# Optimization experiments

Measured on AMD Instinct MI355X. Metric: run time of the kernel, lower is better.

## Reference

```python
import jax, jax.numpy as jnp
import numpy as np

B, L, D, M, R, W = 4, 2048, 2048, 64, 128, 4
SCALE = 1.0 / float(np.sqrt(M))
NORM_EPS = 1e-12


def setup_inputs() -> dict:
    key = jax.random.key(0)
    ks = jax.random.split(key, 8)
    s = lambda k, shape: jax.random.normal(k, shape, jnp.float32) * 0.02
    return dict(
        hidden_states=jax.random.normal(ks[0], (B, L, D), jnp.float32),
        conv_w=s(ks[1], (D, W)),                 # depthwise conv kernel (squeezed [D,1,W])
        conv_b=jnp.zeros((D,), jnp.float32),
        in_proj_w=s(ks[2], (2 * M, D)),          # r,k projection
        ch_gate_w0=s(ks[3], (R, D)),             # low-rank channel gate
        ch_gate_w1=s(ks[4], (D, R)),
        ch_gate_b1=jnp.zeros((D,), jnp.float32),
        mem_gate_w=s(ks[5], (2 * M, D)),         # select/tau gates
        mem_gate_b=jax.random.normal(ks[6], (2 * M,), jnp.float32),
        residual_weight=jnp.ones((D,), jnp.float32),
    )


def _causal_depthwise_conv(x, w, b):
    # x: [B,L,D], w: [D,W], b: [D]; y[t] = sum_i x[t-(W-1)+i] * w[:, i] + b
    xp = jnp.pad(x, ((0, 0), (W - 1, 0), (0, 0)))
    y = sum(xp[:, i:i + x.shape[1], :] * w[:, i] for i in range(W)) + b
    return jax.nn.silu(y)


def reference(hidden_states, conv_w, conv_b, in_proj_w, ch_gate_w0, ch_gate_w1,
              ch_gate_b1, mem_gate_w, mem_gate_b, residual_weight):
    x = hidden_states
    shift = _causal_depthwise_conv(x, conv_w, conv_b)          # [B,L,D]
    residual = shift

    rk = shift @ in_proj_w.T                                   # [B,L,2M]
    r, k = rk[..., :M], rk[..., M:]

    ch = jax.nn.sigmoid((x @ ch_gate_w0.T) @ ch_gate_w1.T + ch_gate_b1)
    u = ch * x                                                 # [B,L,D] gated value

    mg = shift @ mem_gate_w.T + mem_gate_b                     # [B,L,2M]
    sel = jax.nn.softplus(mg[..., :M])
    tau = jax.nn.sigmoid(mg[..., M:])
    it_gate = sel ** tau                                       # input gate
    g = -sel * tau                                             # log decay (rt_gate_log)

    # F.normalize(k) then scale by input gate
    k = k / jnp.maximum(jnp.linalg.norm(k, axis=-1, keepdims=True), NORM_EPS)
    k = k * it_gate

    # GLA recurrence: S_t = diag(exp(g_t)) S_{t-1} + k_t^T u_t; o_t = scale * r_t S_t
    def step(S, inp):
        r_t, k_t, u_t, g_t = inp                               # [B,M],[B,M],[B,D],[B,M]
        S = jnp.exp(g_t)[..., None] * S + k_t[..., None] * u_t[:, None, :]
        o_t = SCALE * jnp.einsum('bm,bmd->bd', r_t, S)
        return S, o_t

    xs = (jnp.swapaxes(r, 0, 1), jnp.swapaxes(k, 0, 1),
          jnp.swapaxes(u, 0, 1), jnp.swapaxes(g, 0, 1))
    S0 = jnp.zeros((x.shape[0], M, D), jnp.float32)
    _, o = jax.lax.scan(step, S0, xs)                          # o: [L,B,D]
    o = jnp.swapaxes(o, 0, 1)

    return o + residual * residual_weight
```

## Files before the change

kernel.cpp:

```cpp
#include <hip/hip_runtime.h>
#include <hip/hip_bf16.h>
#include <math.h>

#define B_ 4
#define L_ 2048
#define D_ 2048
#define M_ 64
#define R_ 128
#define NTOK (B_*L_)
#define SCALE_ 0.125f
#define C_ 32
#define NCH (L_/C_)

typedef __attribute__((ext_vector_type(8))) short short8;
typedef __attribute__((ext_vector_type(4))) float f32x4;

#define BAR() asm volatile("s_waitcnt lgkmcnt(0)\n\ts_barrier" ::: "memory")

#define MFMA(a, b, c) __builtin_amdgcn_mfma_f32_16x16x32_bf16((a), (b), (c), 0, 0, 0)

__device__ __forceinline__ unsigned short f2bfu(float v) {
    union { float f; unsigned u; } a; a.f = v;
    unsigned r = a.u + 0x7fffu + ((a.u >> 16) & 1u);
    return (unsigned short)(r >> 16);
}
__device__ __forceinline__ float bfu2f(unsigned short h) {
    union { unsigned u; float f; } a; a.u = ((unsigned)h) << 16;
    return a.f;
}
__device__ __forceinline__ unsigned pkbf(float a, float b) {
    union { __hip_bfloat162 h; unsigned u; } cv;
    cv.h = __float22bfloat162_rn(make_float2(a, b));
    return cv.u;
}

__global__ __launch_bounds__(256) void k_conv(const float* __restrict__ x,
    const float* __restrict__ cw, const float* __restrict__ cb,
    unsigned short* __restrict__ sh, unsigned short* __restrict__ sl,
    unsigned short* __restrict__ xb)
{
    size_t gid = (size_t)blockIdx.x * 256 + threadIdx.x;
    int dq = (int)(gid & 511);
    size_t tg = gid >> 9;
    int d0 = dq * 4;
    size_t n0 = tg * 8;
    int l0 = (int)(n0 & (L_ - 1));
    const float* xp = x + n0 * D_ + d0;
    float4 w0 = *(const float4*)(cw + (size_t)d0 * 4);
    float4 w1 = *(const float4*)(cw + (size_t)(d0 + 1) * 4);
    float4 w2 = *(const float4*)(cw + (size_t)(d0 + 2) * 4);
    float4 w3 = *(const float4*)(cw + (size_t)(d0 + 3) * 4);
    float4 bias = *(const float4*)(cb + d0);
    float4 v[11];
    if (l0 > 0) {
        v[0] = *(const float4*)(xp - 3 * D_);
        v[1] = *(const float4*)(xp - 2 * D_);
        v[2] = *(const float4*)(xp - 1 * D_);
    } else {
        v[0] = make_float4(0.f, 0.f, 0.f, 0.f);
        v[1] = v[0]; v[2] = v[0];
    }
#pragma unroll
    for (int j = 0; j < 8; j++) v[3 + j] = *(const float4*)(xp + (size_t)j * D_);
#pragma unroll
    for (int j = 0; j < 8; j++) {
        float4 acc = bias;
#pragma unroll
        for (int i = 0; i < 4; i++) {
            float4 xv = v[j + i];
            acc.x = fmaf(xv.x, ((const float*)&w0)[i], acc.x);
            acc.y = fmaf(xv.y, ((const float*)&w1)[i], acc.y);
            acc.z = fmaf(xv.z, ((const float*)&w2)[i], acc.z);
            acc.w = fmaf(xv.w, ((const float*)&w3)[i], acc.w);
        }
        float4 o;
        o.x = acc.x / (1.f + expf(-acc.x));
        o.y = acc.y / (1.f + expf(-acc.y));
        o.z = acc.z / (1.f + expf(-acc.z));
        o.w = acc.w / (1.f + expf(-acc.w));
        ushort4 hv, lv;
        hv.x = f2bfu(o.x); lv.x = f2bfu(o.x - bfu2f(hv.x));
        hv.y = f2bfu(o.y); lv.y = f2bfu(o.y - bfu2f(hv.y));
        hv.z = f2bfu(o.z); lv.z = f2bfu(o.z - bfu2f(hv.z));
        hv.w = f2bfu(o.w); lv.w = f2bfu(o.w - bfu2f(hv.w));
        size_t oo = (n0 + j) * D_ + d0;
        *(ushort4*)(sh + oo) = hv;
        *(ushort4*)(sl + oo) = lv;
        float4 xv = v[3 + j];
        uint2 xpk; xpk.x = pkbf(xv.x, xv.y); xpk.y = pkbf(xv.z, xv.w);
        *(uint2*)(xb + oo) = xpk;
    }
}

__global__ __launch_bounds__(256) void k_castw(
    const float* __restrict__ s0, const float* __restrict__ s1,
    const float* __restrict__ s2, const float* __restrict__ s3,
    unsigned short* __restrict__ d0, unsigned short* __restrict__ d1,
    unsigned short* __restrict__ d2, unsigned short* __restrict__ d3)
{
    int which = blockIdx.x >> 8;
    int idx = ((blockIdx.x & 255) * 256 + threadIdx.x) * 4;
    const float* s = which == 0 ? s0 : which == 1 ? s1 : which == 2 ? s2 : s3;
    unsigned short* d = which == 0 ? d0 : which == 1 ? d1 : which == 2 ? d2 : d3;
    float4 v = *(const float4*)(s + idx);
    uint2 o;
    o.x = pkbf(v.x, v.y);
    o.y = pkbf(v.z, v.w);
    *(uint2*)(d + idx) = o;
}

__global__ __launch_bounds__(256) void k_gemm12(
    const unsigned short* __restrict__ sbf, const unsigned short* __restrict__ xb,
    const unsigned short* __restrict__ Wcatb, const unsigned short* __restrict__ w0b,
    float* __restrict__ rkmg, unsigned short* __restrict__ t1b)
{
    __shared__ __align__(16) unsigned short As[2][64 * 72];
    __shared__ __align__(16) unsigned short Bs[2][64 * 72];
    int tid = threadIdx.x;
    int y = blockIdx.x;
    int n0 = blockIdx.y * 64;
    const unsigned short* A = (y < 4) ? sbf : xb;
    const unsigned short* Bp = (y < 4) ? (Wcatb + (size_t)y * 64 * 2048)
                                       : (w0b + (size_t)(y - 4) * 64 * 2048);
    int wave = tid >> 6, lane = tid & 63;
    int quad = lane >> 4, lcol = lane & 15;
    int wrow = (wave >> 1) * 32, wcol = (wave & 1) * 32;
    int r0 = tid >> 2, sub = (tid & 3) * 8;
    const unsigned short* ap = A + (size_t)(n0 + r0) * 2048 + sub;
    const unsigned short* bp = Bp + (size_t)r0 * 2048 + sub;
    int sidx = r0 * 72 + sub;

    f32x4 acc[2][2];
#pragma unroll
    for (int i = 0; i < 2; i++)
#pragma unroll
        for (int j = 0; j < 2; j++) acc[i][j] = {0.f, 0.f, 0.f, 0.f};

    uint4 av = *(const uint4*)ap;
    uint4 bv = *(const uint4*)bp;
    *(uint4*)&As[0][sidx] = av;
    *(uint4*)&Bs[0][sidx] = bv;
    av = *(const uint4*)(ap + 32);
    bv = *(const uint4*)(bp + 32);
    BAR();

    for (int k32 = 0; k32 < 64; k32++) {
        int cur = k32 & 1;
        short8 af[2], bfr[2];
#pragma unroll
        for (int i = 0; i < 2; i++)
            af[i] = *(short8*)&As[cur][(wrow + i * 16 + lcol) * 72 + quad * 8];
#pragma unroll
        for (int j = 0; j < 2; j++)
            bfr[j] = *(short8*)&Bs[cur][(wcol + j * 16 + lcol) * 72 + quad * 8];
#pragma unroll
        for (int i = 0; i < 2; i++)
#pragma unroll
            for (int j = 0; j < 2; j++)
                acc[i][j] = MFMA(af[i], bfr[j], acc[i][j]);
        if (k32 + 1 < 64) {
            int nb = cur ^ 1;
            *(uint4*)&As[nb][sidx] = av;
            *(uint4*)&Bs[nb][sidx] = bv;
        }
        if (k32 + 2 < 64) {
            int k0 = (k32 + 2) * 32;
            av = *(const uint4*)(ap + k0);
            bv = *(const uint4*)(bp + k0);
        }
        BAR();
    }

#pragma unroll
    for (int i = 0; i < 2; i++)
#pragma unroll
        for (int j = 0; j < 2; j++)
#pragma unroll
            for (int q = 0; q < 4; q++) {
                int row = wrow + i * 16 + quad * 4 + q;
                int col = wcol + j * 16 + lcol;
                int n = n0 + row;
                if (y < 4) rkmg[(size_t)n * 256 + y * 64 + col] = acc[i][j][q];
                else       t1b[(size_t)n * 128 + (y - 4) * 64 + col] = f2bfu(acc[i][j][q]);
            }
}

__global__ __launch_bounds__(256) void k_gemm3(
    const unsigned short* __restrict__ t1b, const unsigned short* __restrict__ w1b,
    const float* __restrict__ b1, const float* __restrict__ x,
    float* __restrict__ u)
{
    __shared__ __align__(16) unsigned short As[2][128 * 32];
    __shared__ __align__(16) unsigned short Bs[2][128 * 32];
    int tid = threadIdx.x;
    int n0 = blockIdx.x * 128;
    int jblk = blockIdx.y * 128;
    int wave = tid >> 6, lane = tid & 63;
    int quad = lane >> 4, lcol = lane & 15;
    int wrow = (wave >> 1) * 64, wcol = (wave & 1) * 64;
    int r0 = tid >> 2;
    int sub = (tid & 3) * 8;
    const unsigned short* a0p = t1b + (size_t)(n0 + r0) * 128 + sub;
    const unsigned short* a1p = t1b + (size_t)(n0 + r0 + 64) * 128 + sub;
    const unsigned short* b0p = w1b + (size_t)(jblk + r0) * 128 + sub;
    const unsigned short* b1p = w1b + (size_t)(jblk + r0 + 64) * 128 + sub;

    f32x4 acc[4][4];
#pragma unroll
    for (int i = 0; i < 4; i++)
#pragma unroll
        for (int j = 0; j < 4; j++) acc[i][j] = {0.f, 0.f, 0.f, 0.f};

    uint4 av0 = *(const uint4*)a0p, av1 = *(const uint4*)a1p;
    uint4 bv0 = *(const uint4*)b0p, bv1 = *(const uint4*)b1p;
    {
        int i0 = tid * 8, i1 = 2048 + tid * 8;
        *(uint4*)&As[0][i0] = av0; *(uint4*)&As[0][i1] = av1;
        *(uint4*)&Bs[0][i0] = bv0; *(uint4*)&Bs[0][i1] = bv1;
    }
    av0 = *(const uint4*)(a0p + 32); av1 = *(const uint4*)(a1p + 32);
    bv0 = *(const uint4*)(b0p + 32); bv1 = *(const uint4*)(b1p + 32);
    BAR();

    for (int k32 = 0; k32 < 4; k32++) {
        int cur = k32 & 1;
        short8 af[4], bfr[4];
#pragma unroll
        for (int i = 0; i < 4; i++)
            af[i] = *(short8*)&As[cur][(wrow + i * 16 + lcol) * 32 + quad * 8];
#pragma unroll
        for (int j = 0; j < 4; j++)
            bfr[j] = *(short8*)&Bs[cur][(wcol + j * 16 + lcol) * 32 + quad * 8];
#pragma unroll
        for (int i = 0; i < 4; i++)
#pragma unroll
            for (int j = 0; j < 4; j++)
                acc[i][j] = MFMA(af[i], bfr[j], acc[i][j]);
        if (k32 + 1 < 4) {
            int nb = cur ^ 1;
            int i0 = tid * 8, i1 = 2048 + tid * 8;
            *(uint4*)&As[nb][i0] = av0; *(uint4*)&As[nb][i1] = av1;
            *(uint4*)&Bs[nb][i0] = bv0; *(uint4*)&Bs[nb][i1] = bv1;
        }
        if (k32 + 2 < 4) {
            int k0 = (k32 + 2) * 32;
            av0 = *(const uint4*)(a0p + k0); av1 = *(const uint4*)(a1p + k0);
            bv0 = *(const uint4*)(b0p + k0); bv1 = *(const uint4*)(b1p + k0);
        }
        BAR();
    }

#pragma unroll
    for (int i = 0; i < 4; i++)
#pragma unroll
        for (int j = 0; j < 4; j++)
#pragma unroll
            for (int q = 0; q < 4; q++) {
                int row = wrow + i * 16 + quad * 4 + q;
                int col = wcol + j * 16 + lcol;
                int n = n0 + row, jc = jblk + col;
                float val = acc[i][j][q] + b1[jc];
                val = 1.f / (1.f + expf(-val));
                val *= x[(size_t)n * D_ + jc];
                u[(size_t)n * D_ + jc] = val;
            }
}

__global__ __launch_bounds__(256) void k_prep(const float* __restrict__ rkmg,
    const float* __restrict__ mb,
    unsigned short* __restrict__ Rt, unsigned short* __restrict__ Kc,
    float* __restrict__ Ac, unsigned short* __restrict__ Pg)
{
    __shared__ float seg[4 * 64];
    __shared__ __align__(16) unsigned short rtL[32 * 72];
    __shared__ __align__(16) unsigned short kdL[32 * 72];
    int blk = blockIdx.x;
    int sg = threadIdx.x >> 6, mm = threadIdx.x & 63;
    int n0 = blk * C_ + sg * 8;

    float rr[8], kk[8], lamr[8];
    float csum = 0.f;
#pragma unroll
    for (int j = 0; j < 8; j++) {
        const float* row = rkmg + (size_t)(n0 + j) * 256;
        float r   = row[mm];
        float k   = row[64 + mm];
        float mg1 = row[128 + mm] + mb[mm];
        float mg2 = row[192 + mm] + mb[64 + mm];
        float sel = (mg1 > 20.f) ? mg1 : log1pf(expf(mg1));
        float tau = 1.f / (1.f + expf(-mg2));
        float it  = expf(tau * logf(sel));
        float g   = -sel * tau;
        float s2  = k * k;
#pragma unroll
        for (int off = 32; off >= 1; off >>= 1) s2 += __shfl_xor(s2, off, 64);
        float kn = k / fmaxf(sqrtf(s2), 1e-12f);
        rr[j] = r;
        kk[j] = kn * it;
        csum += g;
        lamr[j] = csum;
    }
    seg[sg * 64 + mm] = csum;
    __syncthreads();
    float off = 0.f, tot = 0.f;
#pragma unroll
    for (int s = 0; s < 4; s++) {
        float v = seg[s * 64 + mm];
        if (s < sg) off += v;
        tot += v;
    }
    size_t obase = (size_t)blk * (C_ * 64);
    unsigned short kcp[8];
#pragma unroll
    for (int j = 0; j < 8; j++) {
        float lam = off + lamr[j];
        unsigned short rv = f2bfu(rr[j] * expf(lam));
        unsigned short kv = f2bfu(kk[j] * expf(-lam));
        int t = sg * 8 + j;
        Rt[obase + (size_t)t * 64 + mm] = rv;
        rtL[t * 72 + mm] = rv;
        kdL[t * 72 + mm] = kv;
        kcp[j] = f2bfu(kk[j] * expf(tot - lam));
    }
    ushort4 ka4, kb4;
    ka4.x = kcp[0]; ka4.y = kcp[1]; ka4.z = kcp[2]; ka4.w = kcp[3];
    kb4.x = kcp[4]; kb4.y = kcp[5]; kb4.z = kcp[6]; kb4.w = kcp[7];
    *(ushort4*)&Kc[obase + (size_t)mm * C_ + sg * 8]     = ka4;
    *(ushort4*)&Kc[obase + (size_t)mm * C_ + sg * 8 + 4] = kb4;
    if (sg == 0) Ac[(size_t)blk * 64 + mm] = expf(tot);
    __syncthreads();

    int lane = threadIdx.x & 63, quad = lane >> 4, l15 = lane & 15;
    size_t pb = (size_t)blk * 1024;
    if (sg < 3) {
        int ti = (sg == 0) ? 0 : 16;
        int si = (sg == 2) ? 16 : 0;
        short8 a0 = *(const short8*)&rtL[(ti + l15) * 72 + quad * 8];
        short8 a1 = *(const short8*)&rtL[(ti + l15) * 72 + 32 + quad * 8];
        short8 b0 = *(const short8*)&kdL[(si + l15) * 72 + quad * 8];
        short8 b1 = *(const short8*)&kdL[(si + l15) * 72 + 32 + quad * 8];
        f32x4 pp = {0.f, 0.f, 0.f, 0.f};
        pp = MFMA(a0, b0, pp);
        pp = MFMA(a1, b1, pp);
#pragma unroll
        for (int q = 0; q < 4; q++) {
            int t = ti + quad * 4 + q, s = si + l15;
            Pg[pb + t * 32 + s] = f2bfu((s <= t) ? pp[q] : 0.f);
        }
    } else {
#pragma unroll
        for (int q = 0; q < 4; q++)
            Pg[pb + (quad * 4 + q) * 32 + 16 + l15] = 0;
    }
}

#define STAGE(q) do { \
    int t_ = tid >> 3, m8_ = (tid & 7) * 8; \
    *(uint4*)&rtS[q][t_ * 72 + m8_] = rtv; \
    int m_ = tid >> 2, s8_ = (tid & 3) * 8; \
    *(uint4*)&kcS[q][m_ * 40 + s8_] = kcv; \
    int s4_ = (tid & 7) * 4; \
    *(ushort4*)&PlS[q][t_ * 40 + s4_] = plv; \
    int dd_ = tid & 31, tt_ = tid >> 5; \
    _Pragma("unroll") \
    for (int j_ = 0; j_ < 4; j_++) { \
        unsigned short h_ = f2bfu(uv[j_]); \
        UTh[q][dd_ * 40 + tt_ + 8 * j_] = h_; \
        UTl[q][dd_ * 40 + tt_ + 8 * j_] = f2bfu(uv[j_] - bfu2f(h_)); \
    } \
    if (tid < 64) aCs[q][tid] = acv; \
} while (0)

#define PREFETCH(n) do { \
    size_t g_ = cbase + (size_t)(n) * 2048 + (size_t)tid * 8; \
    rtv = *(const uint4*)(Rt + g_); \
    kcv = *(const uint4*)(Kc + g_); \
    plv = *(const ushort4*)(Pg + pbase + (size_t)(n) * 1024 + tid * 4); \
    size_t un_ = ubase + (size_t)(n) * C_ * D_; \
    int dd_ = tid & 31, tt_ = tid >> 5; \
    _Pragma("unroll") \
    for (int j_ = 0; j_ < 4; j_++) \
        uv[j_] = u[un_ + (size_t)(tt_ + 8 * j_) * D_ + dd_]; \
    if (tid < 64) acv = Ac[(size_t)(bNCH + (n)) * 64 + tid]; \
} while (0)

__global__ __launch_bounds__(256) void k_chunk(
    const unsigned short* __restrict__ Rt, const unsigned short* __restrict__ Kc,
    const float* __restrict__ Ac, const unsigned short* __restrict__ Pg,
    const float* __restrict__ u, const unsigned short* __restrict__ sh,
    const unsigned short* __restrict__ sl,
    const float* __restrict__ rw, float* __restrict__ out)
{
    __shared__ __align__(16) unsigned short rtS[2][32 * 72];
    __shared__ __align__(16) unsigned short PlS[2][32 * 40];
    __shared__ __align__(16) unsigned short kcS[2][64 * 40];
    __shared__ __align__(16) unsigned short UTh[2][32 * 40];
    __shared__ __align__(16) unsigned short UTl[2][32 * 40];
    __shared__ __align__(16) unsigned short STh[2][32 * 72];
    __shared__ __align__(16) unsigned short STl[2][32 * 72];
    __shared__ float aCs[2][64];

    int tid = threadIdx.x;
    int wave = tid >> 6, lane = tid & 63;
    int quad = lane >> 4, l15 = lane & 15;
    int b = blockIdx.x & 3, slice = blockIdx.x >> 2;
    int d0 = slice * 32;
    int bNCH = b * NCH;

    for (int i = tid; i < 2 * 32 * 72; i += 256) {
        (&STh[0][0])[i] = 0; (&STl[0][0])[i] = 0;
    }

    size_t cbase = (size_t)b * (L_ * 64);
    size_t pbase = (size_t)bNCH * 1024;
    size_t ubase = (size_t)b * L_ * D_ + d0;

    float rwv = (wave < 2) ? rw[d0 + wave * 16 + l15] : 0.f;

    uint4 rtv, kcv;
    ushort4 plv;
    float uv[4], acv = 0.f;
    unsigned short svh[8], svl[8], svhn[8], svln[8];
    size_t sadr = ubase + (size_t)wave * 16 + l15 + (size_t)(quad * 4) * D_;

    PREFETCH(0);
    STAGE(0);
    PREFETCH(1);
    if (wave < 2) {
#pragma unroll
        for (int tile = 0; tile < 2; tile++)
#pragma unroll
            for (int q = 0; q < 4; q++) {
                svh[tile * 4 + q] = sh[sadr + (size_t)(tile * 16 + q) * D_];
                svl[tile * 4 + q] = sl[sadr + (size_t)(tile * 16 + q) * D_];
            }
    }
    BAR();

    f32x4 zz = {0.f, 0.f, 0.f, 0.f};
    f32x4 sreg[4];
#pragma unroll
    for (int mt = 0; mt < 4; mt++) sreg[mt] = zz;

    for (int c = 0; c < NCH; c++) {
        int p = c & 1;
        if (c + 1 < NCH) STAGE(p ^ 1);
        if (c + 2 < NCH) PREFETCH(c + 2);

        if (wave < 2) {
            if (c + 1 < NCH) {
                size_t s0_ = sadr + (size_t)(c + 1) * C_ * D_;
#pragma unroll
                for (int tile = 0; tile < 2; tile++)
#pragma unroll
                    for (int q = 0; q < 4; q++) {
                        svhn[tile * 4 + q] = sh[s0_ + (size_t)(tile * 16 + q) * D_];
                        svln[tile * 4 + q] = sl[s0_ + (size_t)(tile * 16 + q) * D_];
                    }
            }
            int h = wave;
            short8 a00 = *(const short8*)&rtS[p][l15 * 72 + quad * 8];
            short8 a01 = *(const short8*)&rtS[p][l15 * 72 + 32 + quad * 8];
            short8 a10 = *(const short8*)&rtS[p][(16 + l15) * 72 + quad * 8];
            short8 a11 = *(const short8*)&rtS[p][(16 + l15) * 72 + 32 + quad * 8];
            const unsigned short* sbh = &STh[p ^ 1][(h * 16 + l15) * 72];
            const unsigned short* sbl = &STl[p ^ 1][(h * 16 + l15) * 72];
            short8 sh0 = *(const short8*)&sbh[quad * 8];
            short8 sh1 = *(const short8*)&sbh[32 + quad * 8];
            short8 sl0 = *(const short8*)&sbl[quad * 8];
            short8 sl1 = *(const short8*)&sbl[32 + quad * 8];
            short8 pa0 = *(const short8*)&PlS[p][l15 * 40 + quad * 8];
            short8 pa1 = *(const short8*)&PlS[p][(16 + l15) * 40 + quad * 8];
            short8 uh = *(const short8*)&UTh[p][(h * 16 + l15) * 40 + quad * 8];
            short8 ul = *(const short8*)&UTl[p][(h * 16 + l15) * 40 + quad * 8];
            __builtin_amdgcn_s_setprio(1);
            f32x4 oA0 = MFMA(a00, sh0, zz); oA0 = MFMA(a01, sh1, oA0); oA0 = MFMA(pa0, uh, oA0);
            f32x4 oB0 = MFMA(a00, sl0, zz); oB0 = MFMA(a01, sl1, oB0); oB0 = MFMA(pa0, ul, oB0);
            f32x4 oA1 = MFMA(a10, sh0, zz); oA1 = MFMA(a11, sh1, oA1); oA1 = MFMA(pa1, uh, oA1);
            f32x4 oB1 = MFMA(a10, sl0, zz); oB1 = MFMA(a11, sl1, oB1); oB1 = MFMA(pa1, ul, oB1);
            __builtin_amdgcn_s_setprio(0);
            size_t oa = ubase + (size_t)(c * C_ + quad * 4) * D_ + h * 16 + l15;
#pragma unroll
            for (int q = 0; q < 4; q++) {
                float r0v = bfu2f(svh[q]) + bfu2f(svl[q]);
                float r1v = bfu2f(svh[4 + q]) + bfu2f(svl[4 + q]);
                out[oa + (size_t)q * D_]        = SCALE_ * (oA0[q] + oB0[q]) + r0v * rwv;
                out[oa + (size_t)(16 + q) * D_] = SCALE_ * (oA1[q] + oB1[q]) + r1v * rwv;
            }
#pragma unroll
            for (int q = 0; q < 8; q++) { svh[q] = svhn[q]; svl[q] = svln[q]; }
        } else {
            int h = wave - 2;
            short8 uh = *(const short8*)&UTh[p][(h * 16 + l15) * 40 + quad * 8];
            short8 ul = *(const short8*)&UTl[p][(h * 16 + l15) * 40 + quad * 8];
            __builtin_amdgcn_s_setprio(1);
#pragma unroll
            for (int mt = 0; mt < 4; mt++) {
                f32x4 a4 = *(const f32x4*)&aCs[p][mt * 16 + quad * 4];
                f32x4 s = sreg[mt];
                s[0] *= a4[0]; s[1] *= a4[1]; s[2] *= a4[2]; s[3] *= a4[3];
                short8 ka = *(const short8*)&kcS[p][(mt * 16 + l15) * 40 + quad * 8];
                s = MFMA(ka, uh, s);
                s = MFMA(ka, ul, s);
                sreg[mt] = s;
                unsigned hA = pkbf(s[0], s[1]);
                unsigned hB = pkbf(s[2], s[3]);
                float f0 = bfu2f((unsigned short)hA), f1 = bfu2f((unsigned short)(hA >> 16));
                float f2 = bfu2f((unsigned short)hB), f3 = bfu2f((unsigned short)(hB >> 16));
                unsigned lA = pkbf(s[0] - f0, s[1] - f1);
                unsigned lB = pkbf(s[2] - f2, s[3] - f3);
                int sidx = (h * 16 + l15) * 72 + mt * 16 + quad * 4;
                uint2 wh; wh.x = hA; wh.y = hB;
                uint2 wl; wl.x = lA; wl.y = lB;
                *(uint2*)&STh[p][sidx] = wh;
                *(uint2*)&STl[p][sidx] = wl;
            }
            __builtin_amdgcn_s_setprio(0);
        }
        BAR();
    }
}

extern "C" void kernel_launch(void* const* d_in, const int* in_sizes, int n_in,
                              void* d_out, int out_size, void* d_ws, size_t ws_size,
                              hipStream_t stream)
{
    const float* x   = (const float*)d_in[0];
    const float* cw  = (const float*)d_in[1];
    const float* cb  = (const float*)d_in[2];
    const float* ipw = (const float*)d_in[3];
    const float* w0  = (const float*)d_in[4];
    const float* w1  = (const float*)d_in[5];
    const float* b1  = (const float*)d_in[6];
    const float* mw  = (const float*)d_in[7];
    const float* mb  = (const float*)d_in[8];
    const float* rw  = (const float*)d_in[9];
    float* out = (float*)d_out;

    unsigned short* sh = (unsigned short*)d_ws;
    unsigned short* sl = sh + (size_t)NTOK * D_;
    unsigned short* xb = sl + (size_t)NTOK * D_;
    float* u = (float*)xb;
    float* rkmg = u + (size_t)NTOK * D_;
    float* Ac   = rkmg + (size_t)NTOK * 256;
    unsigned short* Rt  = (unsigned short*)(Ac + (size_t)B_ * NCH * 64);
    unsigned short* Kc  = Rt + (size_t)NTOK * 64;
    unsigned short* Pg  = Kc + (size_t)NTOK * 64;
    unsigned short* t1b = Pg + (size_t)B_ * NCH * 1024;
    unsigned short* Wcatb = t1b + (size_t)NTOK * 128;
    unsigned short* w0b   = Wcatb + 256 * 2048;
    unsigned short* w1b   = w0b + 128 * 2048;

    k_conv<<<(NTOK / 8) * (D_ / 4) / 256, 256, 0, stream>>>(x, cw, cb, sh, sl, xb);

    k_castw<<<1024, 256, 0, stream>>>(ipw, mw, w0, w1,
                                      Wcatb, Wcatb + 128 * 2048, w0b, w1b);

    k_gemm12<<<dim3(6, 128), 256, 0, stream>>>(sh, xb, Wcatb, w0b, rkmg, t1b);

    k_prep<<<B_ * NCH, 256, 0, stream>>>(rkmg, mb, Rt, Kc, Ac, Pg);

    k_gemm3<<<dim3(64, 16), 256, 0, stream>>>(t1b, w1b, b1, x, u);

    k_chunk<<<256, 256, 0, stream>>>(Rt, Kc, Ac, Pg, u, sh, sl, rw, out);
}
```

Before: 284.7 us.

## Halve chunk-scan D slice to double blocks; widen gemm12 K step to 64

```diff
diff --git a/kernel.cpp b/kernel.cpp
--- a/kernel.cpp
+++ b/kernel.cpp
@@ -125,7 +125,7 @@
     int wave = tid >> 6, lane = tid & 63;
     int quad = lane >> 4, lcol = lane & 15;
     int wrow = (wave >> 1) * 32, wcol = (wave & 1) * 32;
-    int r0 = tid >> 2, sub = (tid & 3) * 8;
+    int r0 = tid >> 2, sub = (tid & 3) * 16;
     const unsigned short* ap = A + (size_t)(n0 + r0) * 2048 + sub;
     const unsigned short* bp = Bp + (size_t)r0 * 2048 + sub;
     int sidx = r0 * 72 + sub;
@@ -136,37 +136,38 @@
 #pragma unroll
         for (int j = 0; j < 2; j++) acc[i][j] = {0.f, 0.f, 0.f, 0.f};
 
-    uint4 av = *(const uint4*)ap;
-    uint4 bv = *(const uint4*)bp;
-    *(uint4*)&As[0][sidx] = av;
-    *(uint4*)&Bs[0][sidx] = bv;
-    av = *(const uint4*)(ap + 32);
-    bv = *(const uint4*)(bp + 32);
+    {
+        uint4 a0 = *(const uint4*)ap, a1 = *(const uint4*)(ap + 8);
+        uint4 b0 = *(const uint4*)bp, b1 = *(const uint4*)(bp + 8);
+        *(uint4*)&As[0][sidx] = a0; *(uint4*)&As[0][sidx + 8] = a1;
+        *(uint4*)&Bs[0][sidx] = b0; *(uint4*)&Bs[0][sidx + 8] = b1;
+    }
+    uint4 a0n = *(const uint4*)(ap + 64), a1n = *(const uint4*)(ap + 72);
+    uint4 b0n = *(const uint4*)(bp + 64), b1n = *(const uint4*)(bp + 72);
     BAR();
 
-    for (int k32 = 0; k32 < 64; k32++) {
-        int cur = k32 & 1;
-        short8 af[2], bfr[2];
-#pragma unroll
-        for (int i = 0; i < 2; i++)
-            af[i] = *(short8*)&As[cur][(wrow + i * 16 + lcol) * 72 + quad * 8];
-#pragma unroll
-        for (int j = 0; j < 2; j++)
-            bfr[j] = *(short8*)&Bs[cur][(wcol + j * 16 + lcol) * 72 + quad * 8];
-#pragma unroll
-        for (int i = 0; i < 2; i++)
-#pragma unroll
-            for (int j = 0; j < 2; j++)
-                acc[i][j] = MFMA(af[i], bfr[j], acc[i][j]);
-        if (k32 + 1 < 64) {
+    for (int kk = 0; kk < 32; kk++) {
+        int cur = kk & 1;
+#pragma unroll
+        for (int s = 0; s < 2; s++) {
+            short8 af0 = *(short8*)&As[cur][(wrow + lcol) * 72 + s * 32 + quad * 8];
+            short8 af1 = *(short8*)&As[cur][(wrow + 16 + lcol) * 72 + s * 32 + quad * 8];
+            short8 bf0 = *(short8*)&Bs[cur][(wcol + lcol) * 72 + s * 32 + quad * 8];
+            short8 bf1 = *(short8*)&Bs[cur][(wcol + 16 + lcol) * 72 + s * 32 + quad * 8];
+            acc[0][0] = MFMA(af0, bf0, acc[0][0]);
+            acc[0][1] = MFMA(af0, bf1, acc[0][1]);
+            acc[1][0] = MFMA(af1, bf0, acc[1][0]);
+            acc[1][1] = MFMA(af1, bf1, acc[1][1]);
+        }
+        if (kk + 1 < 32) {
             int nb = cur ^ 1;
-            *(uint4*)&As[nb][sidx] = av;
-            *(uint4*)&Bs[nb][sidx] = bv;
-        }
-        if (k32 + 2 < 64) {
-            int k0 = (k32 + 2) * 32;
-            av = *(const uint4*)(ap + k0);
-            bv = *(const uint4*)(bp + k0);
+            *(uint4*)&As[nb][sidx] = a0n; *(uint4*)&As[nb][sidx + 8] = a1n;
+            *(uint4*)&Bs[nb][sidx] = b0n; *(uint4*)&Bs[nb][sidx + 8] = b1n;
+        }
+        if (kk + 2 < 32) {
+            int k0 = (kk + 2) * 64;
+            a0n = *(const uint4*)(ap + k0); a1n = *(const uint4*)(ap + k0 + 8);
+            b0n = *(const uint4*)(bp + k0); b1n = *(const uint4*)(bp + k0 + 8);
         }
         BAR();
     }
@@ -361,12 +362,12 @@
     *(uint4*)&kcS[q][m_ * 40 + s8_] = kcv; \
     int s4_ = (tid & 7) * 4; \
     *(ushort4*)&PlS[q][t_ * 40 + s4_] = plv; \
-    int dd_ = tid & 31, tt_ = tid >> 5; \
+    int dd_ = tid & 15, tt_ = tid >> 4; \
     _Pragma("unroll") \
-    for (int j_ = 0; j_ < 4; j_++) { \
+    for (int j_ = 0; j_ < 2; j_++) { \
         unsigned short h_ = f2bfu(uv[j_]); \
-        UTh[q][dd_ * 40 + tt_ + 8 * j_] = h_; \
-        UTl[q][dd_ * 40 + tt_ + 8 * j_] = f2bfu(uv[j_] - bfu2f(h_)); \
+        UTh[q][dd_ * 40 + tt_ + 16 * j_] = h_; \
+        UTl[q][dd_ * 40 + tt_ + 16 * j_] = f2bfu(uv[j_] - bfu2f(h_)); \
     } \
     if (tid < 64) aCs[q][tid] = acv; \
 } while (0)
@@ -377,10 +378,9 @@
     kcv = *(const uint4*)(Kc + g_); \
     plv = *(const ushort4*)(Pg + pbase + (size_t)(n) * 1024 + tid * 4); \
     size_t un_ = ubase + (size_t)(n) * C_ * D_; \
-    int dd_ = tid & 31, tt_ = tid >> 5; \
-    _Pragma("unroll") \
-    for (int j_ = 0; j_ < 4; j_++) \
-        uv[j_] = u[un_ + (size_t)(tt_ + 8 * j_) * D_ + dd_]; \
+    int dd_ = tid & 15, tt_ = tid >> 4; \
+    uv[0] = u[un_ + (size_t)tt_ * D_ + dd_]; \
+    uv[1] = u[un_ + (size_t)(tt_ + 16) * D_ + dd_]; \
     if (tid < 64) acv = Ac[(size_t)(bNCH + (n)) * 64 + tid]; \
 } while (0)
 
@@ -394,20 +394,20 @@
     __shared__ __align__(16) unsigned short rtS[2][32 * 72];
     __shared__ __align__(16) unsigned short PlS[2][32 * 40];
     __shared__ __align__(16) unsigned short kcS[2][64 * 40];
-    __shared__ __align__(16) unsigned short UTh[2][32 * 40];
-    __shared__ __align__(16) unsigned short UTl[2][32 * 40];
-    __shared__ __align__(16) unsigned short STh[2][32 * 72];
-    __shared__ __align__(16) unsigned short STl[2][32 * 72];
-    __shared__ float aCs[2][64];
+    __shared__ __align__(16) unsigned short UTh[2][16 * 40];
+    __shared__ __align__(16) unsigned short UTl[2][16 * 40];
+    __shared__ __align__(16) unsigned short STh[2][16 * 72];
+    __shared__ __align__(16) unsigned short STl[2][16 * 72];
+    __shared__ __align__(16) float aCs[2][64];
 
     int tid = threadIdx.x;
     int wave = tid >> 6, lane = tid & 63;
     int quad = lane >> 4, l15 = lane & 15;
     int b = blockIdx.x & 3, slice = blockIdx.x >> 2;
-    int d0 = slice * 32;
+    int d0 = slice * 16;
     int bNCH = b * NCH;
 
-    for (int i = tid; i < 2 * 32 * 72; i += 256) {
+    for (int i = tid; i < 2 * 16 * 72; i += 256) {
         (&STh[0][0])[i] = 0; (&STl[0][0])[i] = 0;
     }
 
@@ -415,32 +415,30 @@
     size_t pbase = (size_t)bNCH * 1024;
     size_t ubase = (size_t)b * L_ * D_ + d0;
 
-    float rwv = (wave < 2) ? rw[d0 + wave * 16 + l15] : 0.f;
+    float rwv = (wave < 2) ? rw[d0 + l15] : 0.f;
+    int ttile = wave;
 
     uint4 rtv, kcv;
     ushort4 plv;
-    float uv[4], acv = 0.f;
-    unsigned short svh[8], svl[8], svhn[8], svln[8];
-    size_t sadr = ubase + (size_t)wave * 16 + l15 + (size_t)(quad * 4) * D_;
+    float uv[2], acv = 0.f;
+    unsigned short svh[4], svl[4], svhn[4], svln[4];
+    size_t sadr = ubase + (size_t)(ttile * 16 + quad * 4) * D_ + l15;
 
     PREFETCH(0);
     STAGE(0);
     PREFETCH(1);
     if (wave < 2) {
 #pragma unroll
-        for (int tile = 0; tile < 2; tile++)
-#pragma unroll
-            for (int q = 0; q < 4; q++) {
-                svh[tile * 4 + q] = sh[sadr + (size_t)(tile * 16 + q) * D_];
-                svl[tile * 4 + q] = sl[sadr + (size_t)(tile * 16 + q) * D_];
-            }
+        for (int q = 0; q < 4; q++) {
+            svh[q] = sh[sadr + (size_t)q * D_];
+            svl[q] = sl[sadr + (size_t)q * D_];
+        }
     }
     BAR();
 
     f32x4 zz = {0.f, 0.f, 0.f, 0.f};
-    f32x4 sreg[4];
-#pragma unroll
-    for (int mt = 0; mt < 4; mt++) sreg[mt] = zz;
+    f32x4 sreg[2];
+    sreg[0] = zz; sreg[1] = zz;
 
     for (int c = 0; c < NCH; c++) {
         int p = c & 1;
@@ -451,65 +449,56 @@
             if (c + 1 < NCH) {
                 size_t s0_ = sadr + (size_t)(c + 1) * C_ * D_;
 #pragma unroll
-                for (int tile = 0; tile < 2; tile++)
-#pragma unroll
-                    for (int q = 0; q < 4; q++) {
-                        svhn[tile * 4 + q] = sh[s0_ + (size_t)(tile * 16 + q) * D_];
-                        svln[tile * 4 + q] = sl[s0_ + (size_t)(tile * 16 + q) * D_];
-                    }
+                for (int q = 0; q < 4; q++) {
+                    svhn[q] = sh[s0_ + (size_t)q * D_];
+                    svln[q] = sl[s0_ + (size_t)q * D_];
+                }
             }
-            int h = wave;
-            short8 a00 = *(const short8*)&rtS[p][l15 * 72 + quad * 8];
-            short8 a01 = *(const short8*)&rtS[p][l15 * 72 + 32 + quad * 8];
-            short8 a10 = *(const short8*)&rtS[p][(16 + l15) * 72 + quad * 8];
-            short8 a11 = *(const short8*)&rtS[p][(16 + l15) * 72 + 32 + quad * 8];
-            const unsigned short* sbh = &STh[p ^ 1][(h * 16 + l15) * 72];
-            const unsigned short* sbl = &STl[p ^ 1][(h * 16 + l15) * 72];
+            short8 a0 = *(const short8*)&rtS[p][(ttile * 16 + l15) * 72 + quad * 8];
+            short8 a1 = *(const short8*)&rtS[p][(ttile * 16 + l15) * 72 + 32 + quad * 8];
+            const unsigned short* sbh = &STh[p ^ 1][l15 * 72];
+            const unsigned short* sbl = &STl[p ^ 1][l15 * 72];
             short8 sh0 = *(const short8*)&sbh[quad * 8];
             short8 sh1 = *(const short8*)&sbh[32 + quad * 8];
             short8 sl0 = *(const short8*)&sbl[quad * 8];
             short8 sl1 = *(const short8*)&sbl[32 + quad * 8];
-            short8 pa0 = *(const short8*)&PlS[p][l15 * 40 + quad * 8];
-            short8 pa1 = *(const short8*)&PlS[p][(16 + l15) * 40 + quad * 8];
-            short8 uh = *(const short8*)&UTh[p][(h * 16 + l15) * 40 + quad * 8];
-            short8 ul = *(const short8*)&UTl[p][(h * 16 + l15) * 40 + quad * 8];
+            short8 pa = *(const short8*)&PlS[p][(ttile * 16 + l15) * 40 + quad * 8];
+            short8 uh = *(const short8*)&UTh[p][l15 * 40 + quad * 8];
+            short8 ul = *(const short8*)&UTl[p][l15 * 40 + quad * 8];
             __builtin_amdgcn_s_setprio(1);
-            f32x4 oA0 = MFMA(a00, sh0, zz); oA0 = MFMA(a01, sh1, oA0); oA0 = MFMA(pa0, uh, oA0);
-            f32x4 oB0 = MFMA(a00, sl0, zz); oB0 = MFMA(a01, sl1, oB0); oB0 = MFMA(pa0, ul, oB0);
-            f32x4 oA1 = MFMA(a10, sh0, zz); oA1 = MFMA(a11, sh1, oA1); oA1 = MFMA(pa1, uh, oA1);
-            f32x4 oB1 = MFMA(a10, sl0, zz); oB1 = MFMA(a11, sl1, oB1); oB1 = MFMA(pa1, ul, oB1);
+            f32x4 oA = MFMA(a0, sh0, zz); oA = MFMA(a1, sh1, oA); oA = MFMA(pa, uh, oA);
+            f32x4 oB = MFMA(a0, sl0, zz); oB = MFMA(a1, sl1, oB); oB = MFMA(pa, ul, oB);
             __builtin_amdgcn_s_setprio(0);
-            size_t oa = ubase + (size_t)(c * C_ + quad * 4) * D_ + h * 16 + l15;
+            size_t oa = ubase + (size_t)(c * C_ + ttile * 16 + quad * 4) * D_ + l15;
 #pragma unroll
             for (int q = 0; q < 4; q++) {
-                float r0v = bfu2f(svh[q]) + bfu2f(svl[q]);
-                float r1v = bfu2f(svh[4 + q]) + bfu2f(svl[4 + q]);
-                out[oa + (size_t)q * D_]        = SCALE_ * (oA0[q] + oB0[q]) + r0v * rwv;
-                out[oa + (size_t)(16 + q) * D_] = SCALE_ * (oA1[q] + oB1[q]) + r1v * rwv;
+                float rv = bfu2f(svh[q]) + bfu2f(svl[q]);
+                out[oa + (size_t)q * D_] = SCALE_ * (oA[q] + oB[q]) + rv * rwv;
             }
 #pragma unroll
-            for (int q = 0; q < 8; q++) { svh[q] = svhn[q]; svl[q] = svln[q]; }
+            for (int q = 0; q < 4; q++) { svh[q] = svhn[q]; svl[q] = svln[q]; }
         } else {
-            int h = wave - 2;
-            short8 uh = *(const short8*)&UTh[p][(h * 16 + l15) * 40 + quad * 8];
-            short8 ul = *(const short8*)&UTl[p][(h * 16 + l15) * 40 + quad * 8];
+            int mt0 = (wave - 2) * 2;
+            short8 uh = *(const short8*)&UTh[p][l15 * 40 + quad * 8];
+            short8 ul = *(const short8*)&UTl[p][l15 * 40 + quad * 8];
             __builtin_amdgcn_s_setprio(1);
 #pragma unroll
-            for (int mt = 0; mt < 4; mt++) {
+            for (int i = 0; i < 2; i++) {
+                int mt = mt0 + i;
                 f32x4 a4 = *(const f32x4*)&aCs[p][mt * 16 + quad * 4];
-                f32x4 s = sreg[mt];
+                f32x4 s = sreg[i];
                 s[0] *= a4[0]; s[1] *= a4[1]; s[2] *= a4[2]; s[3] *= a4[3];
                 short8 ka = *(const short8*)&kcS[p][(mt * 16 + l15) * 40 + quad * 8];
                 s = MFMA(ka, uh, s);
                 s = MFMA(ka, ul, s);
-                sreg[mt] = s;
+                sreg[i] = s;
                 unsigned hA = pkbf(s[0], s[1]);
                 unsigned hB = pkbf(s[2], s[3]);
                 float f0 = bfu2f((unsigned short)hA), f1 = bfu2f((unsigned short)(hA >> 16));
                 float f2 = bfu2f((unsigned short)hB), f3 = bfu2f((unsigned short)(hB >> 16));
                 unsigned lA = pkbf(s[0] - f0, s[1] - f1);
                 unsigned lB = pkbf(s[2] - f2, s[3] - f3);
-                int sidx = (h * 16 + l15) * 72 + mt * 16 + quad * 4;
+                int sidx = l15 * 72 + mt * 16 + quad * 4;
                 uint2 wh; wh.x = hA; wh.y = hB;
                 uint2 wl; wl.x = lA; wl.y = lB;
                 *(uint2*)&STh[p][sidx] = wh;
@@ -562,5 +551,5 @@
 
     k_gemm3<<<dim3(64, 16), 256, 0, stream>>>(t1b, w1b, b1, x, u);
 
-    k_chunk<<<256, 256, 0, stream>>>(Rt, Kc, Ac, Pg, u, sh, sl, rw, out);
-}
+    k_chunk<<<512, 256, 0, stream>>>(Rt, Kc, Ac, Pg, u, sh, sl, rw, out);
+}
```

Result: faster. 278.7 us (-2.1%).
